# Kernel tuning notes

Measured on AMD Instinct MI355X. Metric: run time of the kernel, lower is better.

Reference implementation:

```python
import jax, jax.numpy as jnp
import numpy as np

B, S, F, H, P = 256, 336, 8, 512, 96


def _lstm_step(h, c, x, Wih, Whh, b):
    # PyTorch gate order: input, forget, cell(g), output
    gates = x @ Wih.T + h @ Whh.T + b  # [B, 4H]
    i, f, g, o = jnp.split(gates, 4, axis=-1)
    c_new = jax.nn.sigmoid(f) * c + jax.nn.sigmoid(i) * jnp.tanh(g)
    h_new = jax.nn.sigmoid(o) * jnp.tanh(c_new)
    return h_new, c_new


def setup_inputs() -> dict:
    key = jax.random.key(0)
    ks = jax.random.split(key, 9)
    s_enc = 1.0 / np.sqrt(H)
    return {
        "x_enc": jax.random.normal(ks[0], (B, S, F), jnp.float32),
        "enc_Wih": jax.random.uniform(ks[1], (4 * H, F), jnp.float32, -s_enc, s_enc),
        "enc_Whh": jax.random.uniform(ks[2], (4 * H, H), jnp.float32, -s_enc, s_enc),
        "enc_b": jax.random.uniform(ks[3], (4 * H,), jnp.float32, -s_enc, s_enc),
        "dec_Wih": jax.random.uniform(ks[4], (4 * H, 1), jnp.float32, -s_enc, s_enc),
        "dec_Whh": jax.random.uniform(ks[5], (4 * H, H), jnp.float32, -s_enc, s_enc),
        "dec_b": jax.random.uniform(ks[6], (4 * H,), jnp.float32, -s_enc, s_enc),
        "lin_W": jax.random.uniform(ks[7], (1, H), jnp.float32, -s_enc, s_enc),
        "lin_b": jax.random.uniform(ks[8], (1,), jnp.float32, -s_enc, s_enc),
    }


def reference(x_enc, enc_Wih, enc_Whh, enc_b, dec_Wih, dec_Whh, dec_b, lin_W, lin_b):
    # ---- Encoder: single-layer LSTM over the sequence; keep final (h, c) ----
    def enc_step(carry, x_t):
        h, c = carry
        h, c = _lstm_step(h, c, x_t, enc_Wih, enc_Whh, enc_b)
        return (h, c), None

    h0 = jnp.zeros((B, H), x_enc.dtype)
    c0 = jnp.zeros((B, H), x_enc.dtype)
    xs = jnp.transpose(x_enc, (1, 0, 2))  # [S, B, F]
    (h_enc, c_enc), _ = jax.lax.scan(enc_step, (h0, c0), xs)

    x_dec0 = x_enc[:, -1, 3:4]  # [B, 1] -- feature index 3 of last timestep

    def dec_step(carry, _):
        h, c, x = carry
        h, c = _lstm_step(h, c, x, dec_Wih, dec_Whh, dec_b)
        y = h @ lin_W.T + lin_b  # [B, 1]
        return (h, c, y), y

    _, ys = jax.lax.scan(dec_step, (h_enc, c_enc, x_dec0), None, length=P)
    # ys: [P, B, 1] -> [B, P, 1]
    return jnp.transpose(ys, (1, 0, 2))
```

## Files before the change

### kernel.cpp

```cpp
#include <hip/hip_runtime.h>


typedef _Float16 half8 __attribute__((ext_vector_type(8)));
typedef float f32x4 __attribute__((ext_vector_type(4)));
typedef unsigned long long ull;

#define B_SZ 256
#define S_LEN 336
#define P_LEN 96
#define H_SZ 512
#define T_TOT (S_LEN + P_LEN)

#define SZ_PACK (16*8*17*64*8*2)
#define OFF_PACK_ENC 0
#define OFF_PACK_DEC (SZ_PACK)
#define OFF_HBUF (2*SZ_PACK)
#define SZ_HBUF (2*B_SZ*H_SZ*2)
#define OFF_YBUF (OFF_HBUF + SZ_HBUF)
#define SZ_YBUF (P_LEN*B_SZ*4)
#define OFF_CNT (OFF_YBUF + SZ_YBUF)
#define SZ_CNT (T_TOT*16*4)

__device__ __forceinline__ float sigf(float x){
  return __builtin_amdgcn_rcpf(1.f + __expf(-x));
}
__device__ __forceinline__ float tanh_fast(float x){
  return 2.f*__builtin_amdgcn_rcpf(1.f + __expf(-2.f*x)) - 1.f;
}

__global__ void pack_weights(const float* __restrict__ Whh,
                             const float* __restrict__ Wih,
                             _Float16* __restrict__ dst, int isDec){
  int lane = threadIdx.x;
  int s = blockIdx.x, w = blockIdx.y, og = blockIdx.z;
  int col16 = lane & 15, hi = lane >> 4;
  int gatei = col16 >> 2, uloc = col16 & 3;
  int grow = gatei*H_SZ + og*32 + w*4 + uloc;
  half8 v;
  #pragma unroll
  for (int j = 0; j < 8; j++){
    int k = s*32 + hi*8 + j;
    float x = 0.f;
    if (k < H_SZ)                      x = Whh[(size_t)grow*H_SZ + k];
    else if (!isDec && k < H_SZ + 8)   x = Wih[(size_t)grow*8 + (k - H_SZ)];
    else if (isDec && k == H_SZ)       x = Wih[grow];
    v[j] = (_Float16)x;
  }
  *(half8*)(dst + ((size_t)(((og*8 + w)*17 + s)*64 + lane))*8) = v;
}

__global__ void finalize_out(const float* __restrict__ y_buf,
                             const float* __restrict__ lin_b,
                             float* __restrict__ out){
  int i = blockIdx.x*256 + threadIdx.x;
  int b = i / P_LEN, td = i % P_LEN;
  out[i] = y_buf[td*B_SZ + b] + lin_b[0];
}

#define AFRAG(s) (*(const half8*)&Abuf[abase + (((s)*64 + hi*16) ^ asw)])

__global__ __launch_bounds__(512) void lstm_main(
    const float* __restrict__ x_enc, const float* __restrict__ enc_b,
    const float* __restrict__ dec_b, const float* __restrict__ lin_W,
    const float* __restrict__ lin_b,
    const _Float16* __restrict__ packEnc, const _Float16* __restrict__ packDec,
    ull* __restrict__ h_buf,
    float* __restrict__ y_buf,
    unsigned int* __restrict__ cnt)
{
  const int bx = blockIdx.x;
  const int og = bx >> 4, bg = bx & 15;
  const int tid = threadIdx.x;
  const int w = tid >> 6, lane = tid & 63;
  const int col16 = lane & 15, hi = lane >> 4;
  const int gatei = col16 >> 2;
  const int q4 = col16 & 3;
  const int unit = og*32 + w*4 + q4;
  const int grow = gatei*H_SZ + unit;
  const int r0 = bg*16;

  __shared__ __align__(16) unsigned char Abuf[16*1152];
  __shared__ float yred[8][16];

  half8 Breg[17];
  #pragma unroll
  for (int s = 0; s < 17; s++)
    Breg[s] = *(const half8*)(packEnc + ((size_t)(((og*8 + w)*17 + s)*64 + lane))*8);
  float bias = enc_b[grow];
  const float linw = lin_W[unit];
  const float lbv  = lin_b[0];
  float c4[4] = {0.f, 0.f, 0.f, 0.f};

  const int srow = tid >> 5, sseg = tid & 31;
  const int ssw  = (srow & 7) << 4;
  const int abase = col16*1152;
  const int asw   = (col16 & 7) << 4;

  for (int t = 0; t < T_TOT; t++){
    const bool isDec = (t >= S_LEN);
    if (t == S_LEN){
      #pragma unroll
      for (int s = 0; s < 17; s++)
        Breg[s] = *(const half8*)(packDec + ((size_t)(((og*8 + w)*17 + s)*64 + lane))*8);
      bias = dec_b[grow];
    }

    float xv = 0.f;
    if (!isDec && tid < 128)
      xv = x_enc[(size_t)(r0 + (tid >> 3))*(S_LEN*8) + t*8 + (tid & 7)];

    if (t > 0){
      if (tid == 0){
        while (__hip_atomic_load(&cnt[(t-1)*16 + bg], __ATOMIC_RELAXED,
                                 __HIP_MEMORY_SCOPE_AGENT) != 16u) {}
      }
      __syncthreads();
      const ull* hs = h_buf + ((size_t)(((t-1)&1)*B_SZ + r0 + srow))*128 + sseg*4;
      ull d0 = __hip_atomic_load(hs+0, __ATOMIC_RELAXED, __HIP_MEMORY_SCOPE_AGENT);
      ull d1 = __hip_atomic_load(hs+1, __ATOMIC_RELAXED, __HIP_MEMORY_SCOPE_AGENT);
      ull d2 = __hip_atomic_load(hs+2, __ATOMIC_RELAXED, __HIP_MEMORY_SCOPE_AGENT);
      ull d3 = __hip_atomic_load(hs+3, __ATOMIC_RELAXED, __HIP_MEMORY_SCOPE_AGENT);
      uint4 A;  A.x = (unsigned)d0; A.y = (unsigned)(d0>>32);
                A.z = (unsigned)d1; A.w = (unsigned)(d1>>32);
      uint4 Bv; Bv.x = (unsigned)d2; Bv.y = (unsigned)(d2>>32);
                Bv.z = (unsigned)d3; Bv.w = (unsigned)(d3>>32);
      *(uint4*)&Abuf[srow*1152 + ((sseg*32     ) ^ ssw)] = A;
      *(uint4*)&Abuf[srow*1152 + ((sseg*32 + 16) ^ ssw)] = Bv;
    }

    if (!isDec){
      if (tid < 128){
        int r = tid >> 3, f = tid & 7;
        *(_Float16*)&Abuf[r*1152 + (1024 ^ ((r & 7) << 4)) + f*2] = (_Float16)xv;
      } else if (t == 0 && tid < 176){
        int idx = tid - 128;
        int r = idx & 15, u = (idx >> 4) + 1;
        uint4 z = {0, 0, 0, 0};
        *(uint4*)&Abuf[r*1152 + ((1024 + u*16) ^ ((r & 7) << 4))] = z;
      }
    } else {
      if (tid < 16){
        int r = tid;
        float yv;
        if (t == S_LEN) yv = x_enc[(size_t)(r0 + r)*(S_LEN*8) + 335*8 + 3];
        else yv = __hip_atomic_load(&y_buf[(t-1-S_LEN)*B_SZ + r0 + r],
                                    __ATOMIC_RELAXED, __HIP_MEMORY_SCOPE_AGENT) + lbv;
        half8 va;
        #pragma unroll
        for (int q = 0; q < 8; q++) va[q] = (_Float16)0.f;
        va[0] = (_Float16)yv;
        *(half8*)&Abuf[r*1152 + (1024 ^ ((r & 7) << 4))] = va;
      }
    }
    __syncthreads();

    f32x4 acc = {bias, bias, bias, bias};
    if (t == 0){
      half8 a = AFRAG(16);
      acc = __builtin_amdgcn_mfma_f32_16x16x32_f16(a, Breg[16], acc, 0, 0, 0);
    } else {
      f32x4 acc1 = {0.f, 0.f, 0.f, 0.f};
      #pragma unroll
      for (int s = 0; s < 16; s += 2){
        half8 a0 = AFRAG(s), a1 = AFRAG(s+1);
        acc  = __builtin_amdgcn_mfma_f32_16x16x32_f16(a0, Breg[s],   acc,  0, 0, 0);
        acc1 = __builtin_amdgcn_mfma_f32_16x16x32_f16(a1, Breg[s+1], acc1, 0, 0, 0);
      }
      half8 a16 = AFRAG(16);
      acc = __builtin_amdgcn_mfma_f32_16x16x32_f16(a16, Breg[16], acc, 0, 0, 0);
      acc = acc + acc1;
    }

    float hold[4];
    #pragma unroll
    for (int j = 0; j < 4; j++){
      float a   = acc[j];
      float x4  = __shfl_xor(a, 4);
      float x8  = __shfl_xor(a, 8);
      float x12 = __shfl_xor(x4, 8);
      float gi, gf, gg, go;
      if      (gatei == 0){ gi = a;   gf = x4;  gg = x8;  go = x12; }
      else if (gatei == 1){ gi = x4;  gf = a;   gg = x12; go = x8;  }
      else if (gatei == 2){ gi = x8;  gf = x12; gg = a;   go = x4;  }
      else                { gi = x12; gf = x8;  gg = x4;  go = a;   }
      float cn = sigf(gf)*c4[j] + sigf(gi)*tanh_fast(gg);
      c4[j] = cn;
      hold[j] = sigf(go)*tanh_fast(cn);
    }

    unsigned short s16[4];
    #pragma unroll
    for (int j = 0; j < 4; j++)
      s16[j] = __builtin_bit_cast(unsigned short, (_Float16)hold[j]);
    unsigned lo01 = (unsigned)s16[0] | ((unsigned)s16[1] << 16);
    unsigned hi23 = (unsigned)s16[2] | ((unsigned)s16[3] << 16);
    const bool qlow = (q4 < 2), up = (q4 & 1);
    unsigned sendA = qlow ? hi23 : lo01;
    unsigned rA    = (unsigned)__shfl_xor((int)sendA, 2);
    unsigned keepA = qlow ? lo01 : hi23;
    unsigned vq_p  = up ? (keepA & 0xffffu) : (keepA >> 16);
    unsigned vqx_p = up ? (rA    & 0xffffu) : (rA    >> 16);
    unsigned sendB = qlow ? (vq_p | (vqx_p << 16)) : (vqx_p | (vq_p << 16));
    unsigned rB    = (unsigned)__shfl_xor((int)sendB, 1);
    unsigned vq_m  = up ? (keepA >> 16) : (keepA & 0xffffu);
    unsigned vqx_m = up ? (rA    >> 16) : (rA    & 0xffffu);
    unsigned ownB  = qlow ? (vq_m | (vqx_m << 16)) : (vqx_m | (vq_m << 16));
    unsigned w0 = up ? ((rB & 0xffffu) | (ownB << 16)) : ((ownB & 0xffffu) | (rB << 16));
    unsigned w1 = up ? ((rB >> 16) | (ownB & 0xffff0000u))
                     : ((ownB >> 16) | (rB & 0xffff0000u));
    if (gatei == 0){
      ull hv = (ull)w0 | ((ull)w1 << 32);
      int row = hi*4 + q4;
      __hip_atomic_store(h_buf + ((size_t)((t&1)*B_SZ + r0 + row))*128 + og*8 + w,
                         hv, __ATOMIC_RELAXED, __HIP_MEMORY_SCOPE_AGENT);
    }

    if (isDec){
      #pragma unroll
      for (int j = 0; j < 4; j++){
        float pv = (gatei == 0) ? hold[j]*linw : 0.f;
        pv += __shfl_xor(pv, 1);
        pv += __shfl_xor(pv, 2);
        if (col16 == 0) yred[w][hi*4 + j] = pv;
      }
    }

    asm volatile("s_waitcnt vmcnt(0)" ::: "memory");
    __syncthreads();

    if (isDec && tid < 16){
      float sy = 0.f;
      #pragma unroll
      for (int ww = 0; ww < 8; ww++) sy += yred[ww][tid];
      __hip_atomic_fetch_add(&y_buf[(t-S_LEN)*B_SZ + r0 + tid], sy,
                             __ATOMIC_RELAXED, __HIP_MEMORY_SCOPE_AGENT);
    }
    if (tid == 0){
      asm volatile("s_waitcnt vmcnt(0)" ::: "memory");
      __hip_atomic_fetch_add(&cnt[t*16 + bg], 1u,
                             __ATOMIC_RELAXED, __HIP_MEMORY_SCOPE_AGENT);
    }
  }
}

extern "C" void kernel_launch(void* const* d_in, const int* in_sizes, int n_in,
                              void* d_out, int out_size, void* d_ws, size_t ws_size,
                              hipStream_t stream) {
  const float* x_enc   = (const float*)d_in[0];
  const float* enc_Wih = (const float*)d_in[1];
  const float* enc_Whh = (const float*)d_in[2];
  const float* enc_b   = (const float*)d_in[3];
  const float* dec_Wih = (const float*)d_in[4];
  const float* dec_Whh = (const float*)d_in[5];
  const float* dec_b   = (const float*)d_in[6];
  const float* lin_W   = (const float*)d_in[7];
  const float* lin_b   = (const float*)d_in[8];

  char* ws = (char*)d_ws;
  _Float16* packEnc = (_Float16*)(ws + OFF_PACK_ENC);
  _Float16* packDec = (_Float16*)(ws + OFF_PACK_DEC);
  ull*      h_buf   = (ull*)(ws + OFF_HBUF);
  float*    y_buf   = (float*)(ws + OFF_YBUF);
  unsigned int* cnt = (unsigned int*)(ws + OFF_CNT);

  hipMemsetAsync(ws + OFF_YBUF, 0, SZ_YBUF + SZ_CNT, stream);

  pack_weights<<<dim3(17, 8, 16), 64, 0, stream>>>(enc_Whh, enc_Wih, packEnc, 0);
  pack_weights<<<dim3(17, 8, 16), 64, 0, stream>>>(dec_Whh, dec_Wih, packDec, 1);

  void* args[] = { (void*)&x_enc, (void*)&enc_b, (void*)&dec_b, (void*)&lin_W,
                   (void*)&lin_b, (void*)&packEnc, (void*)&packDec,
                   (void*)&h_buf, (void*)&y_buf, (void*)&cnt };
  hipLaunchCooperativeKernel((void*)lstm_main, dim3(256), dim3(512),
                             args, 0, stream);

  finalize_out<<<dim3((B_SZ*P_LEN)/256), 256, 0, stream>>>(y_buf, lin_b, (float*)d_out);
}
```

Measured before the change: 1.742 ms.

## Fold linear feedback into decoder weights and use per-wave step flags

The decoder's scalar input y = h·linW + b is folded algebraically into a third packed weight set (Whh + Wih·linWᵀ, bias + Wih·lin_b), so decoder steps after the first no longer wait on the y_buf atomic reduction. The per-step group counter with a block-wide barrier is replaced by per-wave monotonic step flags, which every thread polls directly. The LDS A-buffer is double-buffered so the trailing __syncthreads can be dropped. Together these shorten the critical path of each recurrent step. The cost is a third weight pack, heavier polling traffic, and fp16 rounding of the folded weights.

```diff
diff --git a/kernel.cpp b/kernel.cpp
--- a/kernel.cpp
+++ b/kernel.cpp
@@ -12,14 +12,13 @@
 #define T_TOT (S_LEN + P_LEN)
 
 #define SZ_PACK (16*8*17*64*8*2)
-#define OFF_PACK_ENC 0
-#define OFF_PACK_DEC (SZ_PACK)
-#define OFF_HBUF (2*SZ_PACK)
+#define OFF_PACK 0
+#define OFF_HBUF (3*SZ_PACK)
 #define SZ_HBUF (2*B_SZ*H_SZ*2)
 #define OFF_YBUF (OFF_HBUF + SZ_HBUF)
 #define SZ_YBUF (P_LEN*B_SZ*4)
-#define OFF_CNT (OFF_YBUF + SZ_YBUF)
-#define SZ_CNT (T_TOT*16*4)
+#define OFF_FLG (OFF_YBUF + SZ_YBUF)
+#define SZ_FLG (16*128*4)
 
 __device__ __forceinline__ float sigf(float x){
   return __builtin_amdgcn_rcpf(1.f + __expf(-x));
@@ -30,7 +29,8 @@
 
 __global__ void pack_weights(const float* __restrict__ Whh,
                              const float* __restrict__ Wih,
-                             _Float16* __restrict__ dst, int isDec){
+                             const float* __restrict__ linW,
+                             _Float16* __restrict__ dst, int mode){
   int lane = threadIdx.x;
   int s = blockIdx.x, w = blockIdx.y, og = blockIdx.z;
   int col16 = lane & 15, hi = lane >> 4;
@@ -41,9 +41,14 @@
   for (int j = 0; j < 8; j++){
     int k = s*32 + hi*8 + j;
     float x = 0.f;
-    if (k < H_SZ)                      x = Whh[(size_t)grow*H_SZ + k];
-    else if (!isDec && k < H_SZ + 8)   x = Wih[(size_t)grow*8 + (k - H_SZ)];
-    else if (isDec && k == H_SZ)       x = Wih[grow];
+    if (k < H_SZ){
+      x = Whh[(size_t)grow*H_SZ + k];
+      if (mode == 2) x += Wih[grow]*linW[k];
+    } else if (mode == 0 && k < H_SZ + 8){
+      x = Wih[(size_t)grow*8 + (k - H_SZ)];
+    } else if (mode == 1 && k == H_SZ){
+      x = Wih[grow];
+    }
     v[j] = (_Float16)x;
   }
   *(half8*)(dst + ((size_t)(((og*8 + w)*17 + s)*64 + lane))*8) = v;
@@ -57,16 +62,14 @@
   out[i] = y_buf[td*B_SZ + b] + lin_b[0];
 }
 
-#define AFRAG(s) (*(const half8*)&Abuf[abase + (((s)*64 + hi*16) ^ asw)])
-
 __global__ __launch_bounds__(512) void lstm_main(
     const float* __restrict__ x_enc, const float* __restrict__ enc_b,
-    const float* __restrict__ dec_b, const float* __restrict__ lin_W,
-    const float* __restrict__ lin_b,
-    const _Float16* __restrict__ packEnc, const _Float16* __restrict__ packDec,
+    const float* __restrict__ dec_b, const float* __restrict__ dec_Wih,
+    const float* __restrict__ lin_W, const float* __restrict__ lin_b,
+    const _Float16* __restrict__ pack,
     ull* __restrict__ h_buf,
     float* __restrict__ y_buf,
-    unsigned int* __restrict__ cnt)
+    unsigned int* __restrict__ flags)
 {
   const int bx = blockIdx.x;
   const int og = bx >> 4, bg = bx & 15;
@@ -79,42 +82,63 @@
   const int grow = gatei*H_SZ + unit;
   const int r0 = bg*16;
 
-  __shared__ __align__(16) unsigned char Abuf[16*1152];
-  __shared__ float yred[8][16];
+  __shared__ __align__(16) unsigned char Abuf[2][16*1152];
+
+  const _Float16* packBase = pack + ((size_t)((og*8 + w)*17)*64 + lane)*8;
+  const size_t setStride = (size_t)SZ_PACK/2;
 
   half8 Breg[17];
   #pragma unroll
   for (int s = 0; s < 17; s++)
-    Breg[s] = *(const half8*)(packEnc + ((size_t)(((og*8 + w)*17 + s)*64 + lane))*8);
-  float bias = enc_b[grow];
+    Breg[s] = *(const half8*)(packBase + (size_t)s*64*8);
+
+  const float encb = enc_b[grow];
+  const float decb = dec_b[grow];
+  const float wihg = dec_Wih[grow];
   const float linw = lin_W[unit];
   const float lbv  = lin_b[0];
+  float bias = encb;
   float c4[4] = {0.f, 0.f, 0.f, 0.f};
 
   const int srow = tid >> 5, sseg = tid & 31;
   const int ssw  = (srow & 7) << 4;
   const int abase = col16*1152;
   const int asw   = (col16 & 7) << 4;
+  unsigned int* myflags = flags + bg*128;
 
   for (int t = 0; t < T_TOT; t++){
-    const bool isDec = (t >= S_LEN);
+    unsigned char* Ab = Abuf[t & 1];
+
     if (t == S_LEN){
       #pragma unroll
       for (int s = 0; s < 17; s++)
-        Breg[s] = *(const half8*)(packDec + ((size_t)(((og*8 + w)*17 + s)*64 + lane))*8);
-      bias = dec_b[grow];
+        Breg[s] = *(const half8*)(packBase + setStride + (size_t)s*64*8);
+      bias = decb;
+    } else if (t == S_LEN + 1){
+      #pragma unroll
+      for (int s = 0; s < 17; s++)
+        Breg[s] = *(const half8*)(packBase + 2*setStride + (size_t)s*64*8);
+      bias = decb + wihg*lbv;
     }
 
     float xv = 0.f;
-    if (!isDec && tid < 128)
-      xv = x_enc[(size_t)(r0 + (tid >> 3))*(S_LEN*8) + t*8 + (tid & 7)];
+    if (t < S_LEN){
+      if (tid < 128)
+        xv = x_enc[(size_t)(r0 + (tid >> 3))*(S_LEN*8) + t*8 + (tid & 7)];
+    } else if (t == S_LEN){
+      if (tid < 16)
+        xv = x_enc[(size_t)(r0 + tid)*(S_LEN*8) + 335*8 + 3];
+    }
 
     if (t > 0){
-      if (tid == 0){
-        while (__hip_atomic_load(&cnt[(t-1)*16 + bg], __ATOMIC_RELAXED,
-                                 __HIP_MEMORY_SCOPE_AGENT) != 16u) {}
-      }
-      __syncthreads();
+      const ull* fl = (const ull*)myflags + sseg*2;
+      const unsigned tgt = (unsigned)t;
+      for(;;){
+        ull f0 = __hip_atomic_load(fl+0, __ATOMIC_RELAXED, __HIP_MEMORY_SCOPE_AGENT);
+        ull f1 = __hip_atomic_load(fl+1, __ATOMIC_RELAXED, __HIP_MEMORY_SCOPE_AGENT);
+        if ((unsigned)f0 >= tgt && (unsigned)(f0 >> 32) >= tgt &&
+            (unsigned)f1 >= tgt && (unsigned)(f1 >> 32) >= tgt) break;
+      }
       const ull* hs = h_buf + ((size_t)(((t-1)&1)*B_SZ + r0 + srow))*128 + sseg*4;
       ull d0 = __hip_atomic_load(hs+0, __ATOMIC_RELAXED, __HIP_MEMORY_SCOPE_AGENT);
       ull d1 = __hip_atomic_load(hs+1, __ATOMIC_RELAXED, __HIP_MEMORY_SCOPE_AGENT);
@@ -124,50 +148,50 @@
                 A.z = (unsigned)d1; A.w = (unsigned)(d1>>32);
       uint4 Bv; Bv.x = (unsigned)d2; Bv.y = (unsigned)(d2>>32);
                 Bv.z = (unsigned)d3; Bv.w = (unsigned)(d3>>32);
-      *(uint4*)&Abuf[srow*1152 + ((sseg*32     ) ^ ssw)] = A;
-      *(uint4*)&Abuf[srow*1152 + ((sseg*32 + 16) ^ ssw)] = Bv;
-    }
-
-    if (!isDec){
+      *(uint4*)&Ab[srow*1152 + ((sseg*32     ) ^ ssw)] = A;
+      *(uint4*)&Ab[srow*1152 + ((sseg*32 + 16) ^ ssw)] = Bv;
+    }
+
+    if (t < S_LEN){
       if (tid < 128){
         int r = tid >> 3, f = tid & 7;
-        *(_Float16*)&Abuf[r*1152 + (1024 ^ ((r & 7) << 4)) + f*2] = (_Float16)xv;
-      } else if (t == 0 && tid < 176){
-        int idx = tid - 128;
-        int r = idx & 15, u = (idx >> 4) + 1;
+        *(_Float16*)&Ab[r*1152 + (1024 ^ ((r & 7) << 4)) + f*2] = (_Float16)xv;
+      }
+      if (t == 0 && tid >= 256 && tid < 352){
+        int idx = tid - 256;
+        int bsel = idx / 48, rem = idx % 48;
+        int r = rem & 15, u = 1 + (rem >> 4);
         uint4 z = {0, 0, 0, 0};
-        *(uint4*)&Abuf[r*1152 + ((1024 + u*16) ^ ((r & 7) << 4))] = z;
-      }
-    } else {
+        *(uint4*)&Abuf[bsel][r*1152 + ((1024 + u*16) ^ ((r & 7) << 4))] = z;
+      }
+    } else if (t == S_LEN){
       if (tid < 16){
-        int r = tid;
-        float yv;
-        if (t == S_LEN) yv = x_enc[(size_t)(r0 + r)*(S_LEN*8) + 335*8 + 3];
-        else yv = __hip_atomic_load(&y_buf[(t-1-S_LEN)*B_SZ + r0 + r],
-                                    __ATOMIC_RELAXED, __HIP_MEMORY_SCOPE_AGENT) + lbv;
         half8 va;
         #pragma unroll
         for (int q = 0; q < 8; q++) va[q] = (_Float16)0.f;
-        va[0] = (_Float16)yv;
-        *(half8*)&Abuf[r*1152 + (1024 ^ ((r & 7) << 4))] = va;
+        va[0] = (_Float16)xv;
+        *(half8*)&Ab[tid*1152 + (1024 ^ ((tid & 7) << 4))] = va;
       }
     }
     __syncthreads();
 
     f32x4 acc = {bias, bias, bias, bias};
     if (t == 0){
-      half8 a = AFRAG(16);
+      half8 a = *(const half8*)&Ab[abase + ((1024 + hi*16) ^ asw)];
       acc = __builtin_amdgcn_mfma_f32_16x16x32_f16(a, Breg[16], acc, 0, 0, 0);
     } else {
       f32x4 acc1 = {0.f, 0.f, 0.f, 0.f};
       #pragma unroll
       for (int s = 0; s < 16; s += 2){
-        half8 a0 = AFRAG(s), a1 = AFRAG(s+1);
+        half8 a0 = *(const half8*)&Ab[abase + (((s  )*64 + hi*16) ^ asw)];
+        half8 a1 = *(const half8*)&Ab[abase + (((s+1)*64 + hi*16) ^ asw)];
         acc  = __builtin_amdgcn_mfma_f32_16x16x32_f16(a0, Breg[s],   acc,  0, 0, 0);
         acc1 = __builtin_amdgcn_mfma_f32_16x16x32_f16(a1, Breg[s+1], acc1, 0, 0, 0);
       }
-      half8 a16 = AFRAG(16);
-      acc = __builtin_amdgcn_mfma_f32_16x16x32_f16(a16, Breg[16], acc, 0, 0, 0);
+      if (t <= S_LEN){
+        half8 a16 = *(const half8*)&Ab[abase + ((16*64 + hi*16) ^ asw)];
+        acc = __builtin_amdgcn_mfma_f32_16x16x32_f16(a16, Breg[16], acc, 0, 0, 0);
+      }
       acc = acc + acc1;
     }
 
@@ -215,30 +239,21 @@
                          hv, __ATOMIC_RELAXED, __HIP_MEMORY_SCOPE_AGENT);
     }
 
-    if (isDec){
+    asm volatile("s_waitcnt vmcnt(0)" ::: "memory");
+    if (lane == 0)
+      __hip_atomic_store(&myflags[og*8 + w], (unsigned)(t + 1),
+                         __ATOMIC_RELAXED, __HIP_MEMORY_SCOPE_AGENT);
+
+    if (t >= S_LEN){
       #pragma unroll
       for (int j = 0; j < 4; j++){
         float pv = (gatei == 0) ? hold[j]*linw : 0.f;
         pv += __shfl_xor(pv, 1);
         pv += __shfl_xor(pv, 2);
-        if (col16 == 0) yred[w][hi*4 + j] = pv;
-      }
-    }
-
-    asm volatile("s_waitcnt vmcnt(0)" ::: "memory");
-    __syncthreads();
-
-    if (isDec && tid < 16){
-      float sy = 0.f;
-      #pragma unroll
-      for (int ww = 0; ww < 8; ww++) sy += yred[ww][tid];
-      __hip_atomic_fetch_add(&y_buf[(t-S_LEN)*B_SZ + r0 + tid], sy,
-                             __ATOMIC_RELAXED, __HIP_MEMORY_SCOPE_AGENT);
-    }
-    if (tid == 0){
-      asm volatile("s_waitcnt vmcnt(0)" ::: "memory");
-      __hip_atomic_fetch_add(&cnt[t*16 + bg], 1u,
-                             __ATOMIC_RELAXED, __HIP_MEMORY_SCOPE_AGENT);
+        if (col16 == 0)
+          __hip_atomic_fetch_add(&y_buf[(t - S_LEN)*B_SZ + r0 + hi*4 + j], pv,
+                                 __ATOMIC_RELAXED, __HIP_MEMORY_SCOPE_AGENT);
+      }
     }
   }
 }
@@ -257,20 +272,23 @@
   const float* lin_b   = (const float*)d_in[8];
 
   char* ws = (char*)d_ws;
-  _Float16* packEnc = (_Float16*)(ws + OFF_PACK_ENC);
-  _Float16* packDec = (_Float16*)(ws + OFF_PACK_DEC);
-  ull*      h_buf   = (ull*)(ws + OFF_HBUF);
-  float*    y_buf   = (float*)(ws + OFF_YBUF);
-  unsigned int* cnt = (unsigned int*)(ws + OFF_CNT);
-
-  hipMemsetAsync(ws + OFF_YBUF, 0, SZ_YBUF + SZ_CNT, stream);
-
-  pack_weights<<<dim3(17, 8, 16), 64, 0, stream>>>(enc_Whh, enc_Wih, packEnc, 0);
-  pack_weights<<<dim3(17, 8, 16), 64, 0, stream>>>(dec_Whh, dec_Wih, packDec, 1);
-
-  void* args[] = { (void*)&x_enc, (void*)&enc_b, (void*)&dec_b, (void*)&lin_W,
-                   (void*)&lin_b, (void*)&packEnc, (void*)&packDec,
-                   (void*)&h_buf, (void*)&y_buf, (void*)&cnt };
+  _Float16* pack  = (_Float16*)(ws + OFF_PACK);
+  ull*      h_buf = (ull*)(ws + OFF_HBUF);
+  float*    y_buf = (float*)(ws + OFF_YBUF);
+  unsigned int* flags = (unsigned int*)(ws + OFF_FLG);
+
+  hipMemsetAsync(ws + OFF_YBUF, 0, SZ_YBUF + SZ_FLG, stream);
+
+  pack_weights<<<dim3(17, 8, 16), 64, 0, stream>>>(enc_Whh, enc_Wih, lin_W,
+                                                   pack, 0);
+  pack_weights<<<dim3(17, 8, 16), 64, 0, stream>>>(dec_Whh, dec_Wih, lin_W,
+                                                   pack + SZ_PACK/2, 1);
+  pack_weights<<<dim3(17, 8, 16), 64, 0, stream>>>(dec_Whh, dec_Wih, lin_W,
+                                                   pack + SZ_PACK, 2);
+
+  void* args[] = { (void*)&x_enc, (void*)&enc_b, (void*)&dec_b, (void*)&dec_Wih,
+                   (void*)&lin_W, (void*)&lin_b, (void*)&pack,
+                   (void*)&h_buf, (void*)&y_buf, (void*)&flags };
   hipLaunchCooperativeKernel((void*)lstm_main, dim3(256), dim3(512),
                              args, 0, stream);
 
```

Result: slower. 3.494 ms (+100.5%).
